# Optimization experiments

Measured on AMD Instinct MI355X. Metric: run time of the kernel, lower is better.

The kernel has to match this reference:

```python
import jax, jax.numpy as jnp
import numpy as np

B, T, C = 4, 2048, 2048
N_HEAD = 16
HEAD_DIM = C // N_HEAD


def rotate_half(x):
    # interleaved rotate: pairs (x0,x1),(x2,x3),... -> (-x1,x0),(-x3,x2),...
    x1 = x[..., ::2]
    x2 = x[..., 1::2]
    return jnp.stack((-x2, x1), axis=-1).reshape(x.shape)


def compute_rope(seq_len, head_dim, dtype):
    inv_freq = 1.0 / (10000.0 ** (jnp.arange(0, head_dim, 2, dtype=jnp.float32) / head_dim))
    t = jnp.arange(seq_len, dtype=jnp.float32)
    freqs = t[:, None] * inv_freq[None, :]            # [T, head_dim/2]
    emb = jnp.concatenate((freqs, freqs), axis=-1)    # [T, head_dim] (module cats freqs twice)
    cos = jnp.cos(emb)[None, None, :, :].astype(dtype)
    sin = jnp.sin(emb)[None, None, :, :].astype(dtype)
    return cos, sin


def setup_inputs() -> dict:
    key = jax.random.key(0)
    k1, k2, k3, k4, k5 = jax.random.split(key, 5)
    s = 1.0 / np.sqrt(C)
    return {
        "x": jax.random.normal(k1, (B, T, C), dtype=jnp.float32),
        "Wqkv": jax.random.normal(k2, (C, 3 * C), dtype=jnp.float32) * s,
        "bqkv": jnp.zeros((3 * C,), dtype=jnp.float32),
        "Wproj": jax.random.normal(k3, (C, C), dtype=jnp.float32) * s,
        "bproj": jnp.zeros((C,), dtype=jnp.float32),
    }


def reference(x, Wqkv, bqkv, Wproj, bproj):
    Bx, Tx, Cx = x.shape
    qkv = x @ Wqkv + bqkv                              # [B,T,3C]
    q, k, v = jnp.split(qkv, 3, axis=2)
    # -> [B, H, T, D]
    q = q.reshape(Bx, Tx, N_HEAD, HEAD_DIM).transpose(0, 2, 1, 3)
    k = k.reshape(Bx, Tx, N_HEAD, HEAD_DIM).transpose(0, 2, 1, 3)
    v = v.reshape(Bx, Tx, N_HEAD, HEAD_DIM).transpose(0, 2, 1, 3)
    cos, sin = compute_rope(Tx, HEAD_DIM, x.dtype)
    q = q * cos + rotate_half(q) * sin
    k = k * cos + rotate_half(k) * sin
    scale = 1.0 / jnp.sqrt(jnp.asarray(HEAD_DIM, x.dtype))
    scores = jnp.einsum('bhqd,bhkd->bhqk', q, k) * scale
    causal = jnp.tril(jnp.ones((Tx, Tx), dtype=bool))
    scores = jnp.where(causal[None, None, :, :], scores, jnp.asarray(-jnp.inf, x.dtype))
    attn = jax.nn.softmax(scores, axis=-1)
    y = jnp.einsum('bhqk,bhkd->bhqd', attn, v)          # [B,H,T,D]
    y = y.transpose(0, 2, 1, 3).reshape(Bx, Tx, Cx)
    return y @ Wproj + bproj
```

## Files before the change

### kernel.cpp

```cpp
#include <hip/hip_runtime.h>
#include <hip/hip_bf16.h>
#include <stdint.h>

#define DEV __device__ __forceinline__
#define WAITV(n) asm volatile("s_waitcnt vmcnt(" #n ")" ::: "memory")
#define WAITL(n) asm volatile("s_waitcnt lgkmcnt(" #n ")" ::: "memory")
#define SCHEDB __builtin_amdgcn_sched_barrier(0)

typedef __attribute__((ext_vector_type(4))) float f32x4;
typedef __attribute__((ext_vector_type(8))) short bf16x8;
typedef unsigned short u16;

constexpr int Bb = 4, Tt = 2048, Ccn = 2048, NHn = 16, HDn = 128;
constexpr int MM = Bb * Tt;
constexpr int NQKV = 3 * Ccn;
constexpr int KD = 2048;
constexpr size_t K2 = (size_t)KD * 2;
constexpr size_t HKB = 128 * K2;
constexpr float QSCALE = 0.08838834764831845f;

DEV u16 f2bf(float f) {
  __hip_bfloat16 h = __float2bfloat16(f);
  return *reinterpret_cast<u16*>(&h);
}

DEV void gl_lds16(const void* g, void* l) {
  __builtin_amdgcn_global_load_lds(
      (const __attribute__((address_space(1))) void*)g,
      (__attribute__((address_space(3))) void*)l, 16, 0, 0);
}


__global__ void k_rope_table(float* __restrict__ ct, float* __restrict__ st) {
  int idx = blockIdx.x * blockDim.x + threadIdx.x;
  if (idx >= Tt * 64) return;
  int t = idx >> 6, j = idx & 63;
  float invf = expf(-(float)j * 0.14391157f);
  float a = (float)t * invf;
  ct[idx] = cosf(a);
  st[idx] = sinf(a);
}

__global__ void k_cvt(const float* __restrict__ in, u16* __restrict__ out, int n) {
  int i = blockIdx.x * blockDim.x + threadIdx.x;
  int stride = gridDim.x * blockDim.x;
  int n4 = n >> 2;
  for (int idx = i; idx < n4; idx += stride) {
    float4 v = ((const float4*)in)[idx];
    ushort4 o;
    o.x = f2bf(v.x); o.y = f2bf(v.y); o.z = f2bf(v.z); o.w = f2bf(v.w);
    ((ushort4*)out)[idx] = o;
  }
}

__global__ void k_transpose_cvt(const float* __restrict__ in, u16* __restrict__ out,
                                int R, int NC) {
  __shared__ u16 tile[64][72];
  int tr = blockIdx.y * 64, tc = blockIdx.x * 64;
  int r = threadIdx.x >> 2, c = (threadIdx.x & 3) * 16;
  const float* src = in + (size_t)(tr + r) * NC + tc + c;
#pragma unroll
  for (int i = 0; i < 16; i++) tile[r][c + i] = f2bf(src[i]);
  __syncthreads();
  u16* dst = out + (size_t)(tc + r) * R + tr + c;
#pragma unroll
  for (int i = 0; i < 16; i++) dst[i] = tile[c + i][r];
}

__global__ void k_vtrans(const u16* __restrict__ v, u16* __restrict__ vt) {
  __shared__ u16 tile[64][72];
  int bh = blockIdx.z;
  int t0 = blockIdx.x * 64, d0 = blockIdx.y * 64;
  int r = threadIdx.x >> 2, c = (threadIdx.x & 3) * 16;
  const u16* src = v + ((size_t)bh * Tt + t0) * HDn + d0;
#pragma unroll
  for (int i = 0; i < 16; i++) tile[r][c + i] = src[(size_t)r * HDn + c + i];
  __syncthreads();
  u16* dst = vt + ((size_t)bh * HDn + d0) * Tt + t0;
#pragma unroll
  for (int i = 0; i < 16; i++) dst[(size_t)r * Tt + c + i] = tile[c + i][r];
}


template <int MODE>
__global__ __launch_bounds__(512, 2) void k_gemm256(
    const u16* __restrict__ A, const u16* __restrict__ Bt,
    int Ndim, int NBX,
    const float* __restrict__ bias,
    u16* __restrict__ q_r, u16* __restrict__ k_r, u16* __restrict__ v_r,
    const float* __restrict__ ctab, const float* __restrict__ stab,
    float* __restrict__ outp) {
  __shared__ __align__(16) u16 SM[65536];
  const int tid = threadIdx.x;
  const int w = tid >> 6, lane = tid & 63;
  const int l16 = lane & 15, l4 = lane >> 4;
  const int wr = w >> 2, wc = w & 3;
  const int bid = blockIdx.x, nwg = gridDim.x;
  const int swz = (bid & 7) * (nwg >> 3) + (bid >> 3);
  const int by = swz / NBX, bx = swz % NBX;
  const int m0 = by * 256, n0 = bx * 256;
  constexpr int NT = KD >> 6;
  constexpr int NIT = NT >> 1;

  const int Mx = (l16 & 7) << 4;
  const int b6 = Mx & 64;
  const int lane_lo = l16 * 128 + ((l4 * 16) ^ (Mx & 48));
  const char* const pA0 = (const char*)SM + wr * 16384 + lane_lo + b6;
  const char* const pA1 = (const char*)SM + wr * 16384 + lane_lo + (64 - b6);
  const char* const pB0 = (const char*)SM + 65536 + (wc >> 1) * 16384 + (wc & 1) * 8192 + lane_lo + b6;
  const char* const pB1 = (const char*)SM + 65536 + (wc >> 1) * 16384 + (wc & 1) * 8192 + lane_lo + (64 - b6);

  uint32_t soff[2];
#pragma unroll
  for (int i = 0; i < 2; i++) {
    int op = i * 8192 + tid * 16;
    int ol = op ^ (((op >> 7) & 7) << 4);
    int row = ol >> 7, colb = ol & 127;
    soff[i] = (uint32_t)(row * (int)K2 + colb);
  }
  const char* const Ab = (const char*)A + (size_t)m0 * K2;
  const char* const Bbp = (const char*)Bt + (size_t)n0 * K2;
  char* const dstBase = (char*)SM;

  auto stA = [&](int buf, int half, int kt) {
#pragma unroll
    for (int i = 0; i < 2; i++)
      gl_lds16(Ab + (size_t)half * HKB + (size_t)kt * 128 + soff[i],
               dstBase + buf * 32768 + half * 16384 + i * 8192 + tid * 16);
  };
  auto stB = [&](int buf, int half, int kt) {
#pragma unroll
    for (int i = 0; i < 2; i++)
      gl_lds16(Bbp + (size_t)half * HKB + (size_t)kt * 128 + soff[i],
               dstBase + 65536 + buf * 32768 + half * 16384 + i * 8192 + tid * 16);
  };

  bf16x8 af[2][2][2];
  bf16x8 bfr[4][2];
  f32x4 acc[8][4];
  const f32x4 zf = {0.f, 0.f, 0.f, 0.f};
#pragma unroll
  for (int i = 0; i < 8; i++)
#pragma unroll
    for (int j = 0; j < 4; j++) acc[i][j] = zf;

  auto rdAfrag = [&](int par, int bufsel, int ph) {
#pragma unroll
    for (int dm = 0; dm < 2; dm++) {
      af[par][dm][0] = *(const bf16x8*)(pA0 + bufsel * 32768 + (ph * 2 + dm) * 2048);
      af[par][dm][1] = *(const bf16x8*)(pA1 + bufsel * 32768 + (ph * 2 + dm) * 2048);
    }
  };
  auto rdBfrag = [&](int bufsel) {
#pragma unroll
    for (int nj = 0; nj < 4; nj++) {
      bfr[nj][0] = *(const bf16x8*)(pB0 + bufsel * 32768 + nj * 2048);
      bfr[nj][1] = *(const bf16x8*)(pB1 + bufsel * 32768 + nj * 2048);
    }
  };
  auto mfma16 = [&](int par, int ph) {
    __builtin_amdgcn_s_setprio(1);
#pragma unroll
    for (int ks = 0; ks < 2; ks++)
#pragma unroll
      for (int dm = 0; dm < 2; dm++)
#pragma unroll
        for (int nj = 0; nj < 4; nj++)
          acc[ph * 2 + dm][nj] = __builtin_amdgcn_mfma_f32_16x16x32_bf16(
              af[par][dm][ks], bfr[nj][ks], acc[ph * 2 + dm][nj], 0, 0, 0);
    __builtin_amdgcn_s_setprio(0);
  };

  stA(0, 0, 0); stA(0, 1, 0); stB(0, 0, 0); stB(0, 1, 0);
  stB(1, 0, 1); stB(1, 1, 1);
  WAITV(4);
  __builtin_amdgcn_s_barrier();
  SCHEDB;
  rdBfrag(0);
  rdAfrag(0, 0, 0);

  for (int I = 0; I < NIT - 1; ++I) {
    const int t1 = 2 * I + 1, t2 = 2 * I + 2, t3 = 2 * I + 3;
#pragma unroll
    for (int gp = 0; gp < 8; ++gp) {
      __builtin_amdgcn_s_barrier();
      SCHEDB;
      {
        const int ng = (gp + 1) & 7;
        rdAfrag((gp + 1) & 1, ng >> 2, ng & 3);
      }
      if (gp == 0)       stA(1, 0, t1);
      else if (gp == 1)  stA(1, 1, t1);
      else if (gp == 2)  { stB(0, 0, t2); WAITV(2); }
      else if (gp == 3)  stB(0, 1, t2);
      else if (gp == 4)  stA(0, 0, t2);
      else if (gp == 5)  stA(0, 1, t2);
      else if (gp == 6)  { stB(1, 0, t3); WAITV(2); }
      else               stB(1, 1, t3);
      WAITL(4);
      SCHEDB;
      mfma16(gp & 1, gp & 3);
      if (gp == 3)      { rdBfrag(1); SCHEDB; }
      else if (gp == 7) { rdBfrag(0); SCHEDB; }
    }
  }
  {
    const int t1 = 2 * (NIT - 1) + 1;
#pragma unroll
    for (int gp = 0; gp < 8; ++gp) {
      __builtin_amdgcn_s_barrier();
      SCHEDB;
      if (gp < 7) { const int ng = gp + 1; rdAfrag((gp + 1) & 1, ng >> 2, ng & 3); }
      if (gp == 0)       stA(1, 0, t1);
      else if (gp == 1)  stA(1, 1, t1);
      else if (gp == 2)  WAITV(0);
      if (gp == 7) { WAITL(0); } else { WAITL(4); }
      SCHEDB;
      mfma16(gp & 1, gp & 3);
      if (gp == 3) { rdBfrag(1); SCHEDB; }
    }
  }

  if constexpr (MODE == 1) {
#pragma unroll
    for (int mi = 0; mi < 8; mi++) {
      const int mrow = m0 + wr * 128 + mi * 16 + l4 * 4;
#pragma unroll
      for (int nj = 0; nj < 4; nj++) {
        const int col = n0 + wc * 64 + nj * 16 + l16;
        const float bi = bias[col];
#pragma unroll
        for (int jj = 0; jj < 4; jj++)
          outp[(size_t)(mrow + jj) * Ndim + col] = acc[mi][nj][jj] + bi;
      }
    }
  } else {
#pragma unroll
    for (int mi = 0; mi < 8; mi++) {
      const int mrow = m0 + wr * 128 + mi * 16 + l4 * 4;
#pragma unroll
      for (int nj = 0; nj < 4; nj++) {
        const int n = n0 + wc * 64 + nj * 16 + l16;
        const float bi = bias[n];
        const int part = n >> 11;
        const int hcol = n & 2047;
        const int h = hcol >> 7, d = hcol & 127;
        const int dm = d & 63;
#pragma unroll
        for (int jj = 0; jj < 4; jj++) {
          const int m = mrow + jj;
          const int b = m >> 11, t = m & 2047;
          float val = acc[mi][nj][jj] + bi;
          size_t didx = (((size_t)b * NHn + h) * Tt + t) * HDn + d;
          if (part == 2) {
            v_r[didx] = f2bf(val);
          } else {
            float partner = __shfl_xor(val, 1);
            float rh = (d & 1) ? partner : -partner;
            float cs = ctab[t * 64 + dm], sn = stab[t * 64 + dm];
            float o = val * cs + rh * sn;
            if (part == 0) q_r[didx] = f2bf(o * QSCALE);
            else           k_r[didx] = f2bf(o);
          }
        }
      }
    }
  }
}

__global__ __launch_bounds__(256, 2) void k_attn(
    const u16* __restrict__ q_r, const u16* __restrict__ k_r,
    const u16* __restrict__ vt, u16* __restrict__ y) {
  __shared__ u16 Ks[2][64 * 128];
  __shared__ u16 Vs[128 * 64];
  __shared__ u16 Ps[4][32 * 72];
  const int lin = blockIdx.x;
  const int swz = (lin & 7) * 64 + (lin >> 3);
  const int qpair = swz & 7;
  const int bh = swz >> 3;
  const int tid = threadIdx.x, w = tid >> 6, lane = tid & 63;
  const int l16 = lane & 15, l4 = lane >> 4;
  const int b = bh >> 4, h = bh & 15;

  const u16* kbase = k_r + (size_t)bh * Tt * HDn;
  const u16* vbase = vt + (size_t)bh * HDn * Tt;
  const f32x4 zf = {0.f, 0.f, 0.f, 0.f};

  auto stageK = [&](int buf, int j) {
    const char* ksrc = (const char*)(kbase + (size_t)j * 64 * HDn);
#pragma unroll
    for (int i = 0; i < 4; i++) {
      int op = tid * 16 + i * 4096;
      int ol = op ^ (((op >> 8) & 7) << 4);
      gl_lds16(ksrc + ol, (char*)&Ks[buf][0] + op);
    }
  };
  auto stageV = [&](int j) {
    const char* vsrc = (const char*)(vbase + (size_t)j * 64);
#pragma unroll
    for (int i = 0; i < 4; i++) {
      int op = tid * 16 + i * 4096;
      int ol = op ^ (((op >> 7) & 7) << 4);
      int row = ol >> 7, colb = ol & 127;
      gl_lds16(vsrc + (size_t)row * (Tt * 2) + colb, (char*)Vs + op);
    }
  };

#pragma unroll
  for (int qsel = 0; qsel < 2; ++qsel) {
    const int qt = qsel ? (15 - qpair) : qpair;

    const u16* qbase = q_r + ((size_t)bh * Tt + qt * 128 + w * 32) * HDn;
    bf16x8 qf[2][4];
#pragma unroll
    for (int mi = 0; mi < 2; mi++)
#pragma unroll
      for (int kc = 0; kc < 4; kc++)
        qf[mi][kc] = *(const bf16x8*)(qbase + (size_t)(mi * 16 + l16) * HDn + kc * 32 + l4 * 8);

    f32x4 acc_o[2][8];
#pragma unroll
    for (int mi = 0; mi < 2; mi++)
#pragma unroll
      for (int nf = 0; nf < 8; nf++) acc_o[mi][nf] = zf;
    float mrow[2][4], lrow[2][4];
#pragma unroll
    for (int mi = 0; mi < 2; mi++)
#pragma unroll
      for (int jj = 0; jj < 4; jj++) { mrow[mi][jj] = -1e30f; lrow[mi][jj] = 0.f; }

    const int ntiles = 2 * qt + 2;
    stageK(0, 0);
    __syncthreads();
    int cur = 0;

    for (int j = 0; j < ntiles; ++j) {
      const bool more = (j + 1 < ntiles);
      stageV(j);
      if (more) stageK(cur ^ 1, j + 1);

      f32x4 s[2][4];
#pragma unroll
      for (int mi = 0; mi < 2; mi++)
#pragma unroll
        for (int nj = 0; nj < 4; nj++) s[mi][nj] = zf;
#pragma unroll
      for (int kc = 0; kc < 4; kc++) {
        bf16x8 kf[4];
#pragma unroll
        for (int nj = 0; nj < 4; nj++) {
          int row = nj * 16 + l16;
          kf[nj] = *(const bf16x8*)((const char*)&Ks[cur][0] + row * 256 +
                                    ((kc * 64 + l4 * 16) ^ ((row & 7) << 4)));
        }
        __builtin_amdgcn_s_setprio(1);
#pragma unroll
        for (int mi = 0; mi < 2; mi++)
#pragma unroll
          for (int nj = 0; nj < 4; nj++)
            s[mi][nj] = __builtin_amdgcn_mfma_f32_16x16x32_bf16(qf[mi][kc], kf[nj], s[mi][nj], 0, 0, 0);
        __builtin_amdgcn_s_setprio(0);
      }

      const bool diag = (j >= 2 * qt);
#pragma unroll
      for (int mi = 0; mi < 2; mi++) {
#pragma unroll
        for (int jj = 0; jj < 4; jj++) {
          if (diag) {
            const int qrow = qt * 128 + w * 32 + mi * 16 + l4 * 4 + jj;
#pragma unroll
            for (int nj = 0; nj < 4; nj++) {
              const int key = j * 64 + nj * 16 + l16;
              if (key > qrow) s[mi][nj][jj] = -1e30f;
            }
          }
          float lm = fmaxf(fmaxf(s[mi][0][jj], s[mi][1][jj]), fmaxf(s[mi][2][jj], s[mi][3][jj]));
#pragma unroll
          for (int dd = 1; dd < 16; dd <<= 1) lm = fmaxf(lm, __shfl_xor(lm, dd));
          if (lm > mrow[mi][jj]) {
            const float sc = __expf(mrow[mi][jj] - lm);
            mrow[mi][jj] = lm;
            lrow[mi][jj] *= sc;
#pragma unroll
            for (int nf = 0; nf < 8; nf++) acc_o[mi][nf][jj] *= sc;
          }
          float ps = 0.f;
#pragma unroll
          for (int nj = 0; nj < 4; nj++) {
            float p = __expf(s[mi][nj][jj] - mrow[mi][jj]);
            s[mi][nj][jj] = p;
            ps += p;
          }
#pragma unroll
          for (int dd = 1; dd < 16; dd <<= 1) ps += __shfl_xor(ps, dd);
          lrow[mi][jj] += ps;
          const int prow = mi * 16 + l4 * 4 + jj;
#pragma unroll
          for (int nj = 0; nj < 4; nj++)
            Ps[w][prow * 72 + nj * 16 + l16] = f2bf(s[mi][nj][jj]);
        }
      }

      if (more) { WAITV(4); } else { WAITV(0); }
      __builtin_amdgcn_s_barrier();

#pragma unroll
      for (int kc = 0; kc < 2; kc++) {
        bf16x8 pf[2];
#pragma unroll
        for (int mi = 0; mi < 2; mi++)
          pf[mi] = *(const bf16x8*)((const char*)&Ps[w][0] + (mi * 16 + l16) * 144 + kc * 64 + l4 * 16);
        bf16x8 vf[8];
#pragma unroll
        for (int nf = 0; nf < 8; nf++) {
          int row = nf * 16 + l16;
          vf[nf] = *(const bf16x8*)((const char*)Vs + row * 128 +
                                    ((kc * 64 + l4 * 16) ^ ((row & 7) << 4)));
        }
        __builtin_amdgcn_s_setprio(1);
#pragma unroll
        for (int nf = 0; nf < 8; nf++)
#pragma unroll
          for (int mi = 0; mi < 2; mi++)
            acc_o[mi][nf] = __builtin_amdgcn_mfma_f32_16x16x32_bf16(pf[mi], vf[nf], acc_o[mi][nf], 0, 0, 0);
        __builtin_amdgcn_s_setprio(0);
      }
      __syncthreads();
      cur ^= 1;
    }

#pragma unroll
    for (int mi = 0; mi < 2; mi++) {
#pragma unroll
      for (int jj = 0; jj < 4; jj++) {
        const float rinv = 1.f / lrow[mi][jj];
        const int t = qt * 128 + w * 32 + mi * 16 + l4 * 4 + jj;
        u16* yrow = y + ((size_t)b * Tt + t) * Ccn + h * HDn;
#pragma unroll
        for (int nf = 0; nf < 8; nf++)
          yrow[nf * 16 + l16] = f2bf(acc_o[mi][nf][jj] * rinv);
      }
    }
    __syncthreads();
  }
}


extern "C" void kernel_launch(void* const* d_in, const int* in_sizes, int n_in,
                              void* d_out, int out_size, void* d_ws, size_t ws_size,
                              hipStream_t stream) {
  const float* x     = (const float*)d_in[0];
  const float* Wqkv  = (const float*)d_in[1];
  const float* bqkv  = (const float*)d_in[2];
  const float* Wproj = (const float*)d_in[3];
  const float* bproj = (const float*)d_in[4];
  float* out = (float*)d_out;
  char* ws = (char*)d_ws;

  size_t off = 0;
  auto alloc = [&](size_t bytes) -> char* {
    char* p = ws + off;
    off += (bytes + 255) & ~(size_t)255;
    return p;
  };
  float* ctab  = (float*)alloc((size_t)Tt * 64 * sizeof(float));
  float* stab  = (float*)alloc((size_t)Tt * 64 * sizeof(float));
  u16* xb      = (u16*)alloc((size_t)MM * Ccn * 2);
  u16* WqkvT   = (u16*)alloc((size_t)NQKV * Ccn * 2);
  u16* WprojT  = (u16*)alloc((size_t)Ccn * Ccn * 2);
  u16* q_rb    = (u16*)alloc((size_t)MM * Ccn * 2);
  u16* k_rb    = (u16*)alloc((size_t)MM * Ccn * 2);
  u16* v_rb    = (u16*)alloc((size_t)MM * Ccn * 2);
  u16* ybuf    = (u16*)alloc((size_t)MM * Ccn * 2);
  u16* vtb     = xb;

  k_rope_table<<<(Tt * 64 + 255) / 256, 256, 0, stream>>>(ctab, stab);
  k_cvt<<<1024, 256, 0, stream>>>(x, xb, MM * Ccn);
  k_transpose_cvt<<<dim3(NQKV / 64, Ccn / 64), 256, 0, stream>>>(Wqkv, WqkvT, Ccn, NQKV);
  k_transpose_cvt<<<dim3(Ccn / 64, Ccn / 64), 256, 0, stream>>>(Wproj, WprojT, Ccn, Ccn);

  k_gemm256<0><<<dim3((MM / 256) * (NQKV / 256)), 512, 0, stream>>>(
      xb, WqkvT, NQKV, NQKV / 256, bqkv, q_rb, k_rb, v_rb, ctab, stab, nullptr);

  k_vtrans<<<dim3(Tt / 64, HDn / 64, Bb * NHn), 256, 0, stream>>>(v_rb, vtb);

  k_attn<<<dim3(512), 256, 0, stream>>>(q_rb, k_rb, vtb, ybuf);

  k_gemm256<1><<<dim3((MM / 256) * (Ccn / 256)), 512, 0, stream>>>(
      ybuf, WprojT, Ccn, Ccn / 256, bproj, nullptr, nullptr, nullptr, nullptr, nullptr, out);
}
```

Before: 510.1 us.

## Fuse prep kernels, write V transposed in GEMM epilogue, move vmcnt waits

The rope-table, x conversion and two weight transpose-convert kernels are merged into one launch, which removes three launch gaps. The QKV GEMM epilogue now writes V directly in transposed [B,H,D,T] layout with 4-wide stores, so the separate V transpose kernel and its extra round trip through memory go away. The vmcnt waits in the GEMM main loop are moved after the MFMA issue so global-to-LDS loads can overlap more with compute. The transposed V stores are strided by T, which may make the epilogue writes less coalesced.

```diff
diff --git a/kernel.cpp b/kernel.cpp
--- a/kernel.cpp
+++ b/kernel.cpp
@@ -30,55 +30,45 @@
       (__attribute__((address_space(3))) void*)l, 16, 0, 0);
 }
 
-
-__global__ void k_rope_table(float* __restrict__ ct, float* __restrict__ st) {
-  int idx = blockIdx.x * blockDim.x + threadIdx.x;
-  if (idx >= Tt * 64) return;
-  int t = idx >> 6, j = idx & 63;
-  float invf = expf(-(float)j * 0.14391157f);
-  float a = (float)t * invf;
-  ct[idx] = cosf(a);
-  st[idx] = sinf(a);
-}
-
-__global__ void k_cvt(const float* __restrict__ in, u16* __restrict__ out, int n) {
-  int i = blockIdx.x * blockDim.x + threadIdx.x;
-  int stride = gridDim.x * blockDim.x;
-  int n4 = n >> 2;
-  for (int idx = i; idx < n4; idx += stride) {
-    float4 v = ((const float4*)in)[idx];
-    ushort4 o;
-    o.x = f2bf(v.x); o.y = f2bf(v.y); o.z = f2bf(v.z); o.w = f2bf(v.w);
-    ((ushort4*)out)[idx] = o;
-  }
-}
-
-__global__ void k_transpose_cvt(const float* __restrict__ in, u16* __restrict__ out,
-                                int R, int NC) {
+__global__ void k_prep(const float* __restrict__ x, u16* __restrict__ xb,
+                       const float* __restrict__ Wqkv, u16* __restrict__ WqkvT,
+                       const float* __restrict__ Wproj, u16* __restrict__ WprojT,
+                       float* __restrict__ ct, float* __restrict__ st) {
   __shared__ u16 tile[64][72];
-  int tr = blockIdx.y * 64, tc = blockIdx.x * 64;
-  int r = threadIdx.x >> 2, c = (threadIdx.x & 3) * 16;
-  const float* src = in + (size_t)(tr + r) * NC + tc + c;
-#pragma unroll
-  for (int i = 0; i < 16; i++) tile[r][c + i] = f2bf(src[i]);
-  __syncthreads();
-  u16* dst = out + (size_t)(tc + r) * R + tr + c;
-#pragma unroll
-  for (int i = 0; i < 16; i++) dst[i] = tile[c + i][r];
-}
-
-__global__ void k_vtrans(const u16* __restrict__ v, u16* __restrict__ vt) {
-  __shared__ u16 tile[64][72];
-  int bh = blockIdx.z;
-  int t0 = blockIdx.x * 64, d0 = blockIdx.y * 64;
-  int r = threadIdx.x >> 2, c = (threadIdx.x & 3) * 16;
-  const u16* src = v + ((size_t)bh * Tt + t0) * HDn + d0;
-#pragma unroll
-  for (int i = 0; i < 16; i++) tile[r][c + i] = src[(size_t)r * HDn + c + i];
-  __syncthreads();
-  u16* dst = vt + ((size_t)bh * HDn + d0) * Tt + t0;
-#pragma unroll
-  for (int i = 0; i < 16; i++) dst[(size_t)r * Tt + c + i] = tile[c + i][r];
+  const int bid = blockIdx.x, tid = threadIdx.x;
+  if (bid < 1024) {
+    const int n4 = (MM * Ccn) >> 2;
+    for (int idx = bid * 256 + tid; idx < n4; idx += 1024 * 256) {
+      float4 v = ((const float4*)x)[idx];
+      ushort4 o;
+      o.x = f2bf(v.x); o.y = f2bf(v.y); o.z = f2bf(v.z); o.w = f2bf(v.w);
+      ((ushort4*)xb)[idx] = o;
+    }
+  } else if (bid < 5120) {
+    const float* in; u16* out; int NC, bx, by;
+    if (bid < 4096) {
+      int t = bid - 1024; in = Wqkv; out = WqkvT; NC = NQKV; bx = t % 96; by = t / 96;
+    } else {
+      int t = bid - 4096; in = Wproj; out = WprojT; NC = Ccn; bx = t & 31; by = t >> 5;
+    }
+    const int R = 2048;
+    int tr = by * 64, tc = bx * 64;
+    int r = tid >> 2, c = (tid & 3) * 16;
+    const float* src = in + (size_t)(tr + r) * NC + tc + c;
+#pragma unroll
+    for (int i = 0; i < 16; i++) tile[r][c + i] = f2bf(src[i]);
+    __syncthreads();
+    u16* dst = out + (size_t)(tc + r) * R + tr + c;
+#pragma unroll
+    for (int i = 0; i < 16; i++) dst[i] = tile[c + i][r];
+  } else {
+    int idx = (bid - 5120) * 256 + tid;
+    int t = idx >> 6, j = idx & 63;
+    float invf = expf(-(float)j * 0.14391157f);
+    float a = (float)t * invf;
+    ct[idx] = cosf(a);
+    st[idx] = sinf(a);
+  }
 }
 
 
@@ -87,7 +77,7 @@
     const u16* __restrict__ A, const u16* __restrict__ Bt,
     int Ndim, int NBX,
     const float* __restrict__ bias,
-    u16* __restrict__ q_r, u16* __restrict__ k_r, u16* __restrict__ v_r,
+    u16* __restrict__ q_r, u16* __restrict__ k_r, u16* __restrict__ vt,
     const float* __restrict__ ctab, const float* __restrict__ stab,
     float* __restrict__ outp) {
   __shared__ __align__(16) u16 SM[65536];
@@ -191,16 +181,18 @@
       }
       if (gp == 0)       stA(1, 0, t1);
       else if (gp == 1)  stA(1, 1, t1);
-      else if (gp == 2)  { stB(0, 0, t2); WAITV(2); }
+      else if (gp == 2)  stB(0, 0, t2);
       else if (gp == 3)  stB(0, 1, t2);
       else if (gp == 4)  stA(0, 0, t2);
       else if (gp == 5)  stA(0, 1, t2);
-      else if (gp == 6)  { stB(1, 0, t3); WAITV(2); }
+      else if (gp == 6)  stB(1, 0, t3);
       else               stB(1, 1, t3);
       WAITL(4);
       SCHEDB;
       mfma16(gp & 1, gp & 3);
-      if (gp == 3)      { rdBfrag(1); SCHEDB; }
+      if (gp == 2)      { WAITV(2); }
+      else if (gp == 3) { rdBfrag(1); SCHEDB; }
+      else if (gp == 6) { WAITV(2); }
       else if (gp == 7) { rdBfrag(0); SCHEDB; }
     }
   }
@@ -213,11 +205,11 @@
       if (gp < 7) { const int ng = gp + 1; rdAfrag((gp + 1) & 1, ng >> 2, ng & 3); }
       if (gp == 0)       stA(1, 0, t1);
       else if (gp == 1)  stA(1, 1, t1);
-      else if (gp == 2)  WAITV(0);
       if (gp == 7) { WAITL(0); } else { WAITL(4); }
       SCHEDB;
       mfma16(gp & 1, gp & 3);
-      if (gp == 3) { rdBfrag(1); SCHEDB; }
+      if (gp == 2) { WAITV(0); }
+      else if (gp == 3) { rdBfrag(1); SCHEDB; }
     }
   }
 
@@ -238,6 +230,7 @@
 #pragma unroll
     for (int mi = 0; mi < 8; mi++) {
       const int mrow = m0 + wr * 128 + mi * 16 + l4 * 4;
+      const int b = mrow >> 11, t0 = mrow & 2047;
 #pragma unroll
       for (int nj = 0; nj < 4; nj++) {
         const int n = n0 + wc * 64 + nj * 16 + l16;
@@ -246,15 +239,19 @@
         const int hcol = n & 2047;
         const int h = hcol >> 7, d = hcol & 127;
         const int dm = d & 63;
-#pragma unroll
-        for (int jj = 0; jj < 4; jj++) {
-          const int m = mrow + jj;
-          const int b = m >> 11, t = m & 2047;
-          float val = acc[mi][nj][jj] + bi;
-          size_t didx = (((size_t)b * NHn + h) * Tt + t) * HDn + d;
-          if (part == 2) {
-            v_r[didx] = f2bf(val);
-          } else {
+        if (part == 2) {
+          ushort4 vv;
+          vv.x = f2bf(acc[mi][nj][0] + bi);
+          vv.y = f2bf(acc[mi][nj][1] + bi);
+          vv.z = f2bf(acc[mi][nj][2] + bi);
+          vv.w = f2bf(acc[mi][nj][3] + bi);
+          *(ushort4*)(vt + (((size_t)(b * NHn + h)) * HDn + d) * Tt + t0) = vv;
+        } else {
+#pragma unroll
+          for (int jj = 0; jj < 4; jj++) {
+            const int t = t0 + jj;
+            float val = acc[mi][nj][jj] + bi;
+            size_t didx = (((size_t)b * NHn + h) * Tt + t) * HDn + d;
             float partner = __shfl_xor(val, 1);
             float rh = (d & 1) ? partner : -partner;
             float cs = ctab[t * 64 + dm], sn = stab[t * 64 + dm];
@@ -471,19 +468,13 @@
   u16* WprojT  = (u16*)alloc((size_t)Ccn * Ccn * 2);
   u16* q_rb    = (u16*)alloc((size_t)MM * Ccn * 2);
   u16* k_rb    = (u16*)alloc((size_t)MM * Ccn * 2);
-  u16* v_rb    = (u16*)alloc((size_t)MM * Ccn * 2);
+  u16* vtb     = (u16*)alloc((size_t)MM * Ccn * 2);
   u16* ybuf    = (u16*)alloc((size_t)MM * Ccn * 2);
-  u16* vtb     = xb;
-
-  k_rope_table<<<(Tt * 64 + 255) / 256, 256, 0, stream>>>(ctab, stab);
-  k_cvt<<<1024, 256, 0, stream>>>(x, xb, MM * Ccn);
-  k_transpose_cvt<<<dim3(NQKV / 64, Ccn / 64), 256, 0, stream>>>(Wqkv, WqkvT, Ccn, NQKV);
-  k_transpose_cvt<<<dim3(Ccn / 64, Ccn / 64), 256, 0, stream>>>(Wproj, WprojT, Ccn, Ccn);
+
+  k_prep<<<dim3(5632), 256, 0, stream>>>(x, xb, Wqkv, WqkvT, Wproj, WprojT, ctab, stab);
 
   k_gemm256<0><<<dim3((MM / 256) * (NQKV / 256)), 512, 0, stream>>>(
-      xb, WqkvT, NQKV, NQKV / 256, bqkv, q_rb, k_rb, v_rb, ctab, stab, nullptr);
-
-  k_vtrans<<<dim3(Tt / 64, HDn / 64, Bb * NHn), 256, 0, stream>>>(v_rb, vtb);
+      xb, WqkvT, NQKV, NQKV / 256, bqkv, q_rb, k_rb, vtb, ctab, stab, nullptr);
 
   k_attn<<<dim3(512), 256, 0, stream>>>(q_rb, k_rb, vtb, ybuf);
 
```

After: 444.8 us. -12.8%, faster.
